# Optimization experiments

Measured on AMD Instinct MI355X. Metric: run time of the kernel, lower is better.

Reference implementation:

```python
import jax, jax.numpy as jnp
import numpy as np


def setup_inputs() -> dict:
    key = jax.random.key(0)
    kH, kU, kW = jax.random.split(key, 3)
    T, J, D2 = 16384, 1024, 512  # T x 2d context, J x 2d query
    H = jax.random.normal(kH, (T, D2), dtype=jnp.float32)
    U = jax.random.normal(kU, (J, D2), dtype=jnp.float32)
    Ws = jax.random.normal(kW, (3 * D2, 1), dtype=jnp.float32) * 0.05
    return {"H": H, "U": U, "Ws": Ws}


def reference(H, U, Ws):
    D2 = H.shape[-1]
    # Ws applied to concat([H_dup, U_dup, H_dup*U_dup]) decomposes into three blocks.
    w1 = Ws[:D2, 0]          # (2d,)
    w2 = Ws[D2:2 * D2, 0]    # (2d,)
    w3 = Ws[2 * D2:, 0]      # (2d,)
    # Trilinear similarity S[t, j] = H[t]@w1 + U[j]@w2 + (H[t]*U[j])@w3  -> (T, J)
    S = (H @ w1)[:, None] + (U @ w2)[None, :] + (H * w3) @ U.T
    # C2Q attention: softmax over query axis, attend query vectors -> (T, 2d)
    attended_query = jax.nn.softmax(S, axis=-1) @ U
    # Q2C attention: softmax over T of max_j S, rank-1 summary of context -> (2d,)
    b = jax.nn.softmax(jnp.max(S, axis=-1))
    h_tilde = b @ H  # (2d,), tiled to (T, 2d) by broadcasting
    # Merge to query-aware representation G -> (T, 8d)
    G = jnp.concatenate(
        [H, attended_query, H * attended_query, H * h_tilde[None, :]], axis=-1
    )
    return G
```

## Files before the change

### kernel.cpp

```cpp
#include <hip/hip_runtime.h>
#include <hip/hip_bf16.h>

#define T_ROWS 16384
#define J_DIM  1024
#define D_DIM  512

typedef __attribute__((ext_vector_type(8))) short bf16x8;
typedef __attribute__((ext_vector_type(4))) float f32x4;
typedef unsigned short u16;

__device__ __forceinline__ u16 f2bf(float f) {
    union { float f; unsigned int u; } v; v.f = f;
    return (u16)((v.u + 0x7FFFu + ((v.u >> 16) & 1u)) >> 16);
}
__device__ __forceinline__ float bf2f(u16 b) {
    union { unsigned int u; float f; } v; v.u = ((unsigned int)b) << 16;
    return v.f;
}

__device__ __forceinline__ void gload16(const void* g, void* l) {
    __builtin_amdgcn_global_load_lds(
        (__attribute__((address_space(1))) void*)(unsigned long long)(size_t)g,
        (__attribute__((address_space(3))) void*)(unsigned int)(size_t)l,
        16, 0, 0);
}

template<int NT>
__device__ __forceinline__ void gemm_core(
    const u16* A, int lda, const u16* B, int ldb, u16* lds, f32x4 (&acc)[4][4])
{
    const int tid  = threadIdx.x;
    const int lane = tid & 63;
    const int w    = tid >> 6;
    const int wr   = w >> 1, wc = w & 1;
    const int fr   = lane & 15, quad = lane >> 4;

    const int srow = tid >> 2;
    const int ss   = (tid & 3) ^ ((srow >> 1) & 3);

    const u16* gA0 = A + (size_t)srow * lda + ss * 8;
    const u16* gA1 = A + (size_t)(srow + 64) * lda + ss * 8;
    const u16* gB0 = B + (size_t)srow * ldb + ss * 8;
    const u16* gB1 = B + (size_t)(srow + 64) * ldb + ss * 8;

    u16* As = lds;
    u16* Bs = lds + 8192;
    u16* dA0 = As + tid * 8;
    u16* dA1 = As + 2048 + tid * 8;
    u16* dB0 = Bs + tid * 8;
    u16* dB1 = Bs + 2048 + tid * 8;

    gload16(gA0, dA0); gload16(gA1, dA1);
    gload16(gB0, dB0); gload16(gB1, dB1);
    gA0 += 32; gA1 += 32; gB0 += 32; gB1 += 32;

    int offA[4], offB[4];
    #pragma unroll
    for (int i = 0; i < 4; ++i) {
        const int rA = wr * 64 + i * 16 + fr;
        offA[i] = rA * 32 + (quad ^ ((rA >> 1) & 3)) * 8;
        const int rB = wc * 64 + i * 16 + fr;
        offB[i] = rB * 32 + (quad ^ ((rB >> 1) & 3)) * 8;
    }
    __syncthreads();

    #pragma unroll 2
    for (int t = 0; t < NT; ++t) {
        const int cur = (t & 1) * 4096;
        const int nxt = 4096 - cur;
        if (t + 1 < NT) {
            gload16(gA0, dA0 + nxt); gload16(gA1, dA1 + nxt);
            gload16(gB0, dB0 + nxt); gload16(gB1, dB1 + nxt);
            gA0 += 32; gA1 += 32; gB0 += 32; gB1 += 32;
        }
        const u16* Ac = As + cur;
        const u16* Bc = Bs + cur;
        bf16x8 af[4], bfr[4];
        #pragma unroll
        for (int i = 0; i < 4; ++i) af[i]  = *(const bf16x8*)(Ac + offA[i]);
        #pragma unroll
        for (int i = 0; i < 4; ++i) bfr[i] = *(const bf16x8*)(Bc + offB[i]);
        #pragma unroll
        for (int mf = 0; mf < 4; ++mf)
            #pragma unroll
            for (int nf = 0; nf < 4; ++nf)
                acc[mf][nf] = __builtin_amdgcn_mfma_f32_16x16x32_bf16(
                    af[mf], bfr[nf], acc[mf][nf], 0, 0, 0);
        __syncthreads();
    }
}

__global__ __launch_bounds__(256) void prep_kernel(
    const float* __restrict__ H, const float* __restrict__ U,
    const float* __restrict__ Ws,
    float* __restrict__ hw1, float* __restrict__ uw2,
    u16* outU, u16* __restrict__ Ub, u16* __restrict__ Utp)
{
    const int w = threadIdx.x >> 6, lane = threadIdx.x & 63;
    if (blockIdx.x < 4096) {
        const int i = blockIdx.x * 4 + w;
        const float* hp = H + (size_t)i * D_DIM + lane * 8;
        const float4 a = *(const float4*)hp;
        const float4 b = *(const float4*)(hp + 4);
        const float4 w1a = *(const float4*)(Ws + lane * 8);
        const float4 w1b = *(const float4*)(Ws + lane * 8 + 4);
        const float4 w3a = *(const float4*)(Ws + 2 * D_DIM + lane * 8);
        const float4 w3b = *(const float4*)(Ws + 2 * D_DIM + lane * 8 + 4);
        float p = a.x*w1a.x + a.y*w1a.y + a.z*w1a.z + a.w*w1a.w
                + b.x*w1b.x + b.y*w1b.y + b.z*w1b.z + b.w*w1b.w;
        #pragma unroll
        for (int m = 1; m < 64; m <<= 1) p += __shfl_xor(p, m);
        if (lane == 0) hw1[i] = p;
        bf16x8 q;
        q[0] = (short)f2bf(a.x * w3a.x); q[1] = (short)f2bf(a.y * w3a.y);
        q[2] = (short)f2bf(a.z * w3a.z); q[3] = (short)f2bf(a.w * w3a.w);
        q[4] = (short)f2bf(b.x * w3b.x); q[5] = (short)f2bf(b.y * w3b.y);
        q[6] = (short)f2bf(b.z * w3b.z); q[7] = (short)f2bf(b.w * w3b.w);
        *(bf16x8*)(outU + (size_t)i * 4096 + 3072 + lane * 8) = q;
    } else {
        const int j = (blockIdx.x - 4096) * 4 + w;
        const float* up = U + (size_t)j * D_DIM + lane * 8;
        const float4 a = *(const float4*)up;
        const float4 b = *(const float4*)(up + 4);
        const float4 w2a = *(const float4*)(Ws + D_DIM + lane * 8);
        const float4 w2b = *(const float4*)(Ws + D_DIM + lane * 8 + 4);
        float p = a.x*w2a.x + a.y*w2a.y + a.z*w2a.z + a.w*w2a.w
                + b.x*w2b.x + b.y*w2b.y + b.z*w2b.z + b.w*w2b.w;
        #pragma unroll
        for (int m = 1; m < 64; m <<= 1) p += __shfl_xor(p, m);
        if (lane == 0) uw2[j] = p;
        bf16x8 q;
        q[0] = (short)f2bf(a.x); q[1] = (short)f2bf(a.y);
        q[2] = (short)f2bf(a.z); q[3] = (short)f2bf(a.w);
        q[4] = (short)f2bf(b.x); q[5] = (short)f2bf(b.y);
        q[6] = (short)f2bf(b.z); q[7] = (short)f2bf(b.w);
        *(bf16x8*)(Ub + (size_t)j * D_DIM + lane * 8) = q;
        const size_t jpart = (size_t)(j >> 5) * 512
                           + (size_t)(((j >> 3) & 3) * 128) + (j & 7);
        #pragma unroll
        for (int s = 0; s < 8; ++s) {
            const int d = lane * 8 + s;
            Utp[(size_t)(d >> 4) * 16384 + jpart + (size_t)(d & 15) * 8] = (u16)q[s];
        }
    }
}

__global__ __launch_bounds__(256) void s_gemm(
    u16* outU, const u16* __restrict__ Ub, const float* __restrict__ uw2,
    float* __restrict__ pmax)
{
    __shared__ u16 lds[16896];
    __shared__ float redf[256];
    const int bid = blockIdx.x;
    const int swz = (bid & 7) * 128 + (bid >> 3);
    const int bm = swz >> 3, nb = swz & 7;

    f32x4 acc[4][4];
    #pragma unroll
    for (int i = 0; i < 4; ++i)
        #pragma unroll
        for (int j = 0; j < 4; ++j) acc[i][j] = (f32x4){0.f, 0.f, 0.f, 0.f};

    gemm_core<16>(outU + (size_t)bm * 128 * 4096 + 3072, 4096,
                  Ub + (size_t)nb * 128 * 512, 512, lds, acc);

    const int tid = threadIdx.x, lane = tid & 63, w = tid >> 6;
    const int wr = w >> 1, wc = w & 1, fr = lane & 15, quad = lane >> 4;
    float u2[4];
    #pragma unroll
    for (int nf = 0; nf < 4; ++nf) u2[nf] = uw2[nb * 128 + wc * 64 + nf * 16 + fr];

    u16* Tl = lds;
    #pragma unroll
    for (int mf = 0; mf < 4; ++mf)
        #pragma unroll
        for (int m = 0; m < 4; ++m) {
            const int row = wr * 64 + mf * 16 + quad * 4 + m;
            float mv = -1e30f;
            #pragma unroll
            for (int nf = 0; nf < 4; ++nf) {
                acc[mf][nf][m] += u2[nf];
                mv = fmaxf(mv, acc[mf][nf][m]);
            }
            mv = fmaxf(mv, __shfl_xor(mv, 1));
            mv = fmaxf(mv, __shfl_xor(mv, 2));
            mv = fmaxf(mv, __shfl_xor(mv, 4));
            mv = fmaxf(mv, __shfl_xor(mv, 8));
            if (fr == 0) redf[wc * 128 + row] = mv;
            #pragma unroll
            for (int nf = 0; nf < 4; ++nf)
                Tl[row * 132 + wc * 64 + nf * 16 + fr] = f2bf(acc[mf][nf][m]);
        }
    __syncthreads();

    if (wc == 0 && fr == 0) {
        #pragma unroll
        for (int mf = 0; mf < 4; ++mf)
            #pragma unroll
            for (int m = 0; m < 4; ++m) {
                const int rr = wr * 64 + mf * 16 + quad * 4 + m;
                pmax[((size_t)bm * 128 + rr) * 8 + nb] =
                    fmaxf(redf[rr], redf[128 + rr]);
            }
    }

    {
        const int rr = tid >> 1, hf = tid & 1;
        const u16* src = Tl + rr * 132 + hf * 64;
        u16* dst = outU + (size_t)(bm * 128 + rr) * 4096 + 1024 + nb * 128 + hf * 64;
        #pragma unroll
        for (int i = 0; i < 8; ++i)
            *(bf16x8*)(dst + i * 8) = *(const bf16x8*)(src + i * 8);
    }
}

__global__ __launch_bounds__(512) void bh_kernel(
    const float* __restrict__ pmax, const float* __restrict__ hw1,
    const float* __restrict__ H, float* __restrict__ part)
{
    const int b = blockIdx.x;
    const int t = threadIdx.x;
    __shared__ float red8[8];
    __shared__ float esh[64];
    __shared__ float Msh, Lsh;

    float rs[32];
    float m = -1e30f;
    #pragma unroll
    for (int k = 0; k < 32; ++k) {
        const int r = t + k * 512;
        const float4 p0 = *(const float4*)(pmax + (size_t)r * 8);
        const float4 p1 = *(const float4*)(pmax + (size_t)r * 8 + 4);
        rs[k] = fmaxf(fmaxf(fmaxf(p0.x, p0.y), fmaxf(p0.z, p0.w)),
                      fmaxf(fmaxf(p1.x, p1.y), fmaxf(p1.z, p1.w))) + hw1[r];
        m = fmaxf(m, rs[k]);
    }
    #pragma unroll
    for (int s = 1; s < 64; s <<= 1) m = fmaxf(m, __shfl_xor(m, s));
    if ((t & 63) == 0) red8[t >> 6] = m;
    __syncthreads();
    if (t == 0) {
        float M = red8[0];
        #pragma unroll
        for (int i = 1; i < 8; ++i) M = fmaxf(M, red8[i]);
        Msh = M;
    }
    __syncthreads();
    const float M = Msh;
    float l = 0.f;
    #pragma unroll
    for (int k = 0; k < 32; ++k) l += __expf(rs[k] - M);
    #pragma unroll
    for (int s = 1; s < 64; s <<= 1) l += __shfl_xor(l, s);
    if ((t & 63) == 0) red8[t >> 6] = l;
    __syncthreads();
    if (t == 0) {
        float L = 0.f;
        #pragma unroll
        for (int i = 0; i < 8; ++i) L += red8[i];
        Lsh = L;
    }
    __syncthreads();
    const float invL = 1.f / Lsh;

    if (t < 64) {
        const int r = b * 64 + t;
        const float4 p0 = *(const float4*)(pmax + (size_t)r * 8);
        const float4 p1 = *(const float4*)(pmax + (size_t)r * 8 + 4);
        const float rsv = fmaxf(fmaxf(fmaxf(p0.x, p0.y), fmaxf(p0.z, p0.w)),
                                fmaxf(fmaxf(p1.x, p1.y), fmaxf(p1.z, p1.w))) + hw1[r];
        esh[t] = __expf(rsv - M) * invL;
    }
    __syncthreads();

    float s = 0.f;
    const float* hp = H + (size_t)b * 64 * D_DIM + t;
    #pragma unroll 8
    for (int ri = 0; ri < 64; ++ri)
        s += esh[ri] * hp[(size_t)ri * D_DIM];
    part[(size_t)b * D_DIM + t] = s;
}

__global__ __launch_bounds__(512) void htilde_reduce(
    const float* __restrict__ part, float* __restrict__ ht)
{
    const int d = threadIdx.x;
    float s = 0.f;
    for (int p = 0; p < 256; ++p) s += part[(size_t)p * D_DIM + d];
    ht[d] = s;
}

__global__ __launch_bounds__(512, 4) void pv_fused(
    u16* outU, const u16* __restrict__ Utp, const float* __restrict__ H,
    const float* __restrict__ htld)
{
    __shared__ float SPf[32 * 520];
    u16* SP = (u16*)SPf;
    const int tid = threadIdx.x, lane = tid & 63, w = tid >> 6;
    const int fr = lane & 15, quad = lane >> 4;
    const int ib = blockIdx.x * 32;

    #pragma unroll
    for (int p = 0; p < 8; ++p) {
        const int slot = p * 512 + tid;
        const int r  = slot >> 7;
        const int c8 = slot & 127;
        gload16(outU + (size_t)(ib + r) * 4096 + 1024 + (size_t)((c8 ^ (r & 7)) * 8),
                SP + (size_t)slot * 8);
    }
    __syncthreads();

    #pragma unroll
    for (int rr = 0; rr < 4; ++rr) {
        const int r = w * 4 + rr;
        u16* row = SP + (size_t)r * 1024;
        const int s0 = (lane ^ (r & 7)) * 8;
        const int s1 = ((lane + 64) ^ (r & 7)) * 8;
        bf16x8 x0 = *(bf16x8*)(row + s0);
        bf16x8 x1 = *(bf16x8*)(row + s1);
        float f0[8], f1[8];
        float mx = -1e30f;
        #pragma unroll
        for (int i = 0; i < 8; ++i) {
            f0[i] = bf2f((u16)x0[i]); f1[i] = bf2f((u16)x1[i]);
            mx = fmaxf(mx, fmaxf(f0[i], f1[i]));
        }
        #pragma unroll
        for (int s = 1; s < 64; s <<= 1) mx = fmaxf(mx, __shfl_xor(mx, s));
        float sum = 0.f;
        #pragma unroll
        for (int i = 0; i < 8; ++i) {
            f0[i] = __expf(f0[i] - mx); f1[i] = __expf(f1[i] - mx);
            sum += f0[i] + f1[i];
        }
        #pragma unroll
        for (int s = 1; s < 64; s <<= 1) sum += __shfl_xor(sum, s);
        const float inv = 1.f / sum;
        bf16x8 y0, y1;
        #pragma unroll
        for (int i = 0; i < 8; ++i) {
            y0[i] = (short)f2bf(f0[i] * inv);
            y1[i] = (short)f2bf(f1[i] * inv);
        }
        *(bf16x8*)(row + s0) = y0;
        *(bf16x8*)(row + s1) = y1;
    }
    __syncthreads();

    f32x4 acc[2][4];
    #pragma unroll
    for (int i = 0; i < 2; ++i)
        #pragma unroll
        for (int j = 0; j < 4; ++j) acc[i][j] = (f32x4){0.f, 0.f, 0.f, 0.f};

    const u16* bp = Utp + (size_t)lane * 8;
    bf16x8 bA[4], bB[4];
    #pragma unroll
    for (int nf = 0; nf < 4; ++nf)
        bA[nf] = *(const bf16x8*)(bp + ((size_t)(w * 4 + nf) * 32) * 512);

    for (int ks = 0; ks < 32; ks += 2) {
        #pragma unroll
        for (int nf = 0; nf < 4; ++nf)
            bB[nf] = *(const bf16x8*)(bp + ((size_t)(w * 4 + nf) * 32 + ks + 1) * 512);
        bf16x8 a0[2];
        #pragma unroll
        for (int mf = 0; mf < 2; ++mf)
            a0[mf] = *(const bf16x8*)(SP + (size_t)(mf * 16 + fr) * 1024
                                         + (size_t)(((ks * 4 + quad) ^ (fr & 7)) * 8));
        __builtin_amdgcn_s_setprio(1);
        #pragma unroll
        for (int mf = 0; mf < 2; ++mf)
            #pragma unroll
            for (int nf = 0; nf < 4; ++nf)
                acc[mf][nf] = __builtin_amdgcn_mfma_f32_16x16x32_bf16(
                    a0[mf], bA[nf], acc[mf][nf], 0, 0, 0);
        __builtin_amdgcn_s_setprio(0);
        if (ks + 2 < 32) {
            #pragma unroll
            for (int nf = 0; nf < 4; ++nf)
                bA[nf] = *(const bf16x8*)(bp + ((size_t)(w * 4 + nf) * 32 + ks + 2) * 512);
        }
        bf16x8 a1[2];
        #pragma unroll
        for (int mf = 0; mf < 2; ++mf)
            a1[mf] = *(const bf16x8*)(SP + (size_t)(mf * 16 + fr) * 1024
                                         + (size_t)((((ks + 1) * 4 + quad) ^ (fr & 7)) * 8));
        __builtin_amdgcn_s_setprio(1);
        #pragma unroll
        for (int mf = 0; mf < 2; ++mf)
            #pragma unroll
            for (int nf = 0; nf < 4; ++nf)
                acc[mf][nf] = __builtin_amdgcn_mfma_f32_16x16x32_bf16(
                    a1[mf], bB[nf], acc[mf][nf], 0, 0, 0);
        __builtin_amdgcn_s_setprio(0);
    }
    __syncthreads();

    #pragma unroll
    for (int mf = 0; mf < 2; ++mf)
        #pragma unroll
        for (int m = 0; m < 4; ++m) {
            const int r = mf * 16 + quad * 4 + m;
            #pragma unroll
            for (int nf = 0; nf < 4; ++nf)
                SPf[r * 520 + w * 64 + nf * 16 + fr] = acc[mf][nf][m];
        }
    __syncthreads();

    {
        const int r = tid >> 4;
        const int l16 = tid & 15;
        const size_t grow = (size_t)ib + r;
        const float* hrow = H + grow * D_DIM;
        float* ob = (float*)outU + grow * 2048;
        #pragma unroll
        for (int i = 0; i < 8; ++i) {
            const int c = l16 * 4 + i * 64;
            const float4 h  = *(const float4*)(hrow + c);
            const float4 aq = *(const float4*)(&SPf[r * 520 + c]);
            const float4 hv = *(const float4*)(htld + c);
            float4 ha, hh;
            ha.x = h.x * aq.x; ha.y = h.y * aq.y; ha.z = h.z * aq.z; ha.w = h.w * aq.w;
            hh.x = h.x * hv.x; hh.y = h.y * hv.y; hh.z = h.z * hv.z; hh.w = h.w * hv.w;
            *(float4*)(ob + c)        = h;
            *(float4*)(ob + 512 + c)  = aq;
            *(float4*)(ob + 1024 + c) = ha;
            *(float4*)(ob + 1536 + c) = hh;
        }
    }
}

extern "C" void kernel_launch(void* const* d_in, const int* in_sizes, int n_in,
                              void* d_out, int out_size, void* d_ws, size_t ws_size,
                              hipStream_t stream)
{
    const float* H  = (const float*)d_in[0];
    const float* U  = (const float*)d_in[1];
    const float* Ws = (const float*)d_in[2];
    u16* outU = (u16*)d_out;

    float* uw2   = (float*)d_ws;
    float* hw1   = uw2 + 1024;
    float* htld  = hw1 + T_ROWS;
    float* part  = htld + D_DIM;
    float* pmax  = part + 256 * D_DIM;
    u16*   Ub    = (u16*)(pmax + (size_t)T_ROWS * 8);
    u16*   Utp   = Ub + (size_t)J_DIM * D_DIM;

    hipLaunchKernelGGL(prep_kernel, dim3(4096 + 256), dim3(256), 0, stream,
                       H, U, Ws, hw1, uw2, outU, Ub, Utp);
    hipLaunchKernelGGL(s_gemm, dim3(1024), dim3(256), 0, stream,
                       outU, Ub, uw2, pmax);
    hipLaunchKernelGGL(bh_kernel, dim3(256), dim3(512), 0, stream,
                       pmax, hw1, H, part);
    hipLaunchKernelGGL(htilde_reduce, dim3(1), dim3(512), 0, stream, part, htld);
    hipLaunchKernelGGL(pv_fused, dim3(T_ROWS / 32), dim3(512), 0, stream,
                       outU, Utp, H, htld);
}
```

Measured before the change: 133.4 us.

## Fuse Q2C softmax and h-tilde reduction into PV kernel via atomic flags

After: 286.1 us. +114.5%, slower.

```diff
diff --git a/kernel.cpp b/kernel.cpp
--- a/kernel.cpp
+++ b/kernel.cpp
@@ -94,8 +94,10 @@
     const float* __restrict__ H, const float* __restrict__ U,
     const float* __restrict__ Ws,
     float* __restrict__ hw1, float* __restrict__ uw2,
-    u16* outU, u16* __restrict__ Ub, u16* __restrict__ Utp)
+    u16* outU, u16* __restrict__ Ub, u16* __restrict__ Utp,
+    unsigned* __restrict__ ctr)
 {
+    if (blockIdx.x == 0 && threadIdx.x == 0) { ctr[0] = 0u; ctr[1] = 0u; }
     const int w = threadIdx.x >> 6, lane = threadIdx.x & 63;
     if (blockIdx.x < 4096) {
         const int i = blockIdx.x * 4 + w;
@@ -214,91 +216,97 @@
     }
 }
 
-__global__ __launch_bounds__(512) void bh_kernel(
+__global__ __launch_bounds__(512, 4) void pv_mega(
+    u16* outU, const u16* __restrict__ Utp, const float* __restrict__ H,
     const float* __restrict__ pmax, const float* __restrict__ hw1,
-    const float* __restrict__ H, float* __restrict__ part)
+    float* __restrict__ part, float* __restrict__ htld,
+    unsigned* __restrict__ ctr)
 {
-    const int b = blockIdx.x;
-    const int t = threadIdx.x;
+    __shared__ float SPf[32 * 520];
     __shared__ float red8[8];
     __shared__ float esh[64];
     __shared__ float Msh, Lsh;
-
-    float rs[32];
-    float m = -1e30f;
-    #pragma unroll
-    for (int k = 0; k < 32; ++k) {
-        const int r = t + k * 512;
-        const float4 p0 = *(const float4*)(pmax + (size_t)r * 8);
-        const float4 p1 = *(const float4*)(pmax + (size_t)r * 8 + 4);
-        rs[k] = fmaxf(fmaxf(fmaxf(p0.x, p0.y), fmaxf(p0.z, p0.w)),
-                      fmaxf(fmaxf(p1.x, p1.y), fmaxf(p1.z, p1.w))) + hw1[r];
-        m = fmaxf(m, rs[k]);
-    }
-    #pragma unroll
-    for (int s = 1; s < 64; s <<= 1) m = fmaxf(m, __shfl_xor(m, s));
-    if ((t & 63) == 0) red8[t >> 6] = m;
-    __syncthreads();
-    if (t == 0) {
-        float M = red8[0];
-        #pragma unroll
-        for (int i = 1; i < 8; ++i) M = fmaxf(M, red8[i]);
-        Msh = M;
-    }
-    __syncthreads();
-    const float M = Msh;
-    float l = 0.f;
-    #pragma unroll
-    for (int k = 0; k < 32; ++k) l += __expf(rs[k] - M);
-    #pragma unroll
-    for (int s = 1; s < 64; s <<= 1) l += __shfl_xor(l, s);
-    if ((t & 63) == 0) red8[t >> 6] = l;
-    __syncthreads();
-    if (t == 0) {
-        float L = 0.f;
-        #pragma unroll
-        for (int i = 0; i < 8; ++i) L += red8[i];
-        Lsh = L;
-    }
-    __syncthreads();
-    const float invL = 1.f / Lsh;
-
-    if (t < 64) {
-        const int r = b * 64 + t;
-        const float4 p0 = *(const float4*)(pmax + (size_t)r * 8);
-        const float4 p1 = *(const float4*)(pmax + (size_t)r * 8 + 4);
-        const float rsv = fmaxf(fmaxf(fmaxf(p0.x, p0.y), fmaxf(p0.z, p0.w)),
-                                fmaxf(fmaxf(p1.x, p1.y), fmaxf(p1.z, p1.w))) + hw1[r];
-        esh[t] = __expf(rsv - M) * invL;
-    }
-    __syncthreads();
-
-    float s = 0.f;
-    const float* hp = H + (size_t)b * 64 * D_DIM + t;
-    #pragma unroll 8
-    for (int ri = 0; ri < 64; ++ri)
-        s += esh[ri] * hp[(size_t)ri * D_DIM];
-    part[(size_t)b * D_DIM + t] = s;
-}
-
-__global__ __launch_bounds__(512) void htilde_reduce(
-    const float* __restrict__ part, float* __restrict__ ht)
-{
-    const int d = threadIdx.x;
-    float s = 0.f;
-    for (int p = 0; p < 256; ++p) s += part[(size_t)p * D_DIM + d];
-    ht[d] = s;
-}
-
-__global__ __launch_bounds__(512, 4) void pv_fused(
-    u16* outU, const u16* __restrict__ Utp, const float* __restrict__ H,
-    const float* __restrict__ htld)
-{
-    __shared__ float SPf[32 * 520];
     u16* SP = (u16*)SPf;
     const int tid = threadIdx.x, lane = tid & 63, w = tid >> 6;
     const int fr = lane & 15, quad = lane >> 4;
-    const int ib = blockIdx.x * 32;
+    const int bid = blockIdx.x;
+    const int ib = bid * 32;
+    volatile unsigned* vctr = ctr;
+
+    if (bid < 256) {
+        float rs[32];
+        float m = -1e30f;
+        #pragma unroll
+        for (int k = 0; k < 32; ++k) {
+            const int r = tid + k * 512;
+            const float4 p0 = *(const float4*)(pmax + (size_t)r * 8);
+            const float4 p1 = *(const float4*)(pmax + (size_t)r * 8 + 4);
+            rs[k] = fmaxf(fmaxf(fmaxf(p0.x, p0.y), fmaxf(p0.z, p0.w)),
+                          fmaxf(fmaxf(p1.x, p1.y), fmaxf(p1.z, p1.w))) + hw1[r];
+            m = fmaxf(m, rs[k]);
+        }
+        #pragma unroll
+        for (int s = 1; s < 64; s <<= 1) m = fmaxf(m, __shfl_xor(m, s));
+        if ((tid & 63) == 0) red8[tid >> 6] = m;
+        __syncthreads();
+        if (tid == 0) {
+            float M = red8[0];
+            #pragma unroll
+            for (int i = 1; i < 8; ++i) M = fmaxf(M, red8[i]);
+            Msh = M;
+        }
+        __syncthreads();
+        const float M = Msh;
+        float l = 0.f;
+        #pragma unroll
+        for (int k = 0; k < 32; ++k) l += __expf(rs[k] - M);
+        #pragma unroll
+        for (int s = 1; s < 64; s <<= 1) l += __shfl_xor(l, s);
+        if ((tid & 63) == 0) red8[tid >> 6] = l;
+        __syncthreads();
+        if (tid == 0) {
+            float L = 0.f;
+            #pragma unroll
+            for (int i = 0; i < 8; ++i) L += red8[i];
+            Lsh = L;
+        }
+        __syncthreads();
+        const float invL = 1.f / Lsh;
+
+        if (tid < 64) {
+            const int r = bid * 64 + tid;
+            const float4 p0 = *(const float4*)(pmax + (size_t)r * 8);
+            const float4 p1 = *(const float4*)(pmax + (size_t)r * 8 + 4);
+            const float rsv = fmaxf(fmaxf(fmaxf(p0.x, p0.y), fmaxf(p0.z, p0.w)),
+                                    fmaxf(fmaxf(p1.x, p1.y), fmaxf(p1.z, p1.w))) + hw1[r];
+            esh[tid] = __expf(rsv - M) * invL;
+        }
+        __syncthreads();
+
+        float s = 0.f;
+        const float* hp = H + (size_t)bid * 64 * D_DIM + tid;
+        #pragma unroll 8
+        for (int ri = 0; ri < 64; ++ri)
+            s += esh[ri] * hp[(size_t)ri * D_DIM];
+        part[(size_t)bid * D_DIM + tid] = s;
+        __threadfence();
+        __syncthreads();
+        if (tid == 0) atomicAdd(&ctr[0], 1u);
+    }
+
+    if (bid == 511) {
+        if (tid == 0) {
+            while (vctr[0] < 256u) __builtin_amdgcn_s_sleep(8);
+        }
+        __syncthreads();
+        __threadfence();
+        float s = 0.f;
+        for (int p = 0; p < 256; ++p) s += part[(size_t)p * D_DIM + tid];
+        htld[tid] = s;
+        __threadfence();
+        __syncthreads();
+        if (tid == 0) atomicExch(&ctr[1], 1u);
+    }
 
     #pragma unroll
     for (int p = 0; p < 8; ++p) {
@@ -406,7 +414,12 @@
             for (int nf = 0; nf < 4; ++nf)
                 SPf[r * 520 + w * 64 + nf * 16 + fr] = acc[mf][nf][m];
         }
-    __syncthreads();
+
+    if (tid == 0) {
+        while (vctr[1] == 0u) __builtin_amdgcn_s_sleep(8);
+    }
+    __syncthreads();
+    __threadfence();
 
     {
         const int r = tid >> 4;
@@ -445,16 +458,14 @@
     float* htld  = hw1 + T_ROWS;
     float* part  = htld + D_DIM;
     float* pmax  = part + 256 * D_DIM;
-    u16*   Ub    = (u16*)(pmax + (size_t)T_ROWS * 8);
+    unsigned* ctr = (unsigned*)(pmax + (size_t)T_ROWS * 8);
+    u16*   Ub    = (u16*)(ctr + 4);
     u16*   Utp   = Ub + (size_t)J_DIM * D_DIM;
 
     hipLaunchKernelGGL(prep_kernel, dim3(4096 + 256), dim3(256), 0, stream,
-                       H, U, Ws, hw1, uw2, outU, Ub, Utp);
+                       H, U, Ws, hw1, uw2, outU, Ub, Utp, ctr);
     hipLaunchKernelGGL(s_gemm, dim3(1024), dim3(256), 0, stream,
                        outU, Ub, uw2, pmax);
-    hipLaunchKernelGGL(bh_kernel, dim3(256), dim3(512), 0, stream,
-                       pmax, hw1, H, part);
-    hipLaunchKernelGGL(htilde_reduce, dim3(1), dim3(512), 0, stream, part, htld);
-    hipLaunchKernelGGL(pv_fused, dim3(T_ROWS / 32), dim3(512), 0, stream,
-                       outU, Utp, H, htld);
-}
+    hipLaunchKernelGGL(pv_mega, dim3(T_ROWS / 32), dim3(512), 0, stream,
+                       outU, Utp, H, pmax, hw1, part, htld, ctr);
+}
```
